# Kernel tuning notes

Hardware: AMD Instinct MI355X
Metric: run time of the kernel (lower is better)

## Reference

```python
import jax, jax.numpy as jnp
import numpy as np

B, NS, S, H = 512, 2, 128, 768
DS, NL = 384, 40
TEMP, ALPHA, GAMMA = 0.05, 0.15, 7.5
EPS = 1e-8


def setup_inputs() -> dict:
    key = jax.random.key(0)
    ks = jax.random.split(key, 8)
    return {
        "bert_emb": jax.random.normal(ks[0], (B, NS, S, H), dtype=jnp.float32),
        "rel_desc_emb": jax.random.normal(ks[1], (B, DS), dtype=jnp.float32),
        "dense_w": 0.02 * jax.random.normal(ks[2], (H, H), dtype=jnp.float32),
        "dense_b": jnp.zeros((H,), dtype=jnp.float32),
        "cls_w": 0.02 * jax.random.normal(ks[3], (3 * H, NL), dtype=jnp.float32),
        "cls_b": jnp.zeros((NL,), dtype=jnp.float32),
        "fc_w": 0.02 * jax.random.normal(ks[4], (3 * H, DS), dtype=jnp.float32),
        "fc_b": jnp.zeros((DS,), dtype=jnp.float32),
        "entity_idx": jax.random.randint(ks[5], (B, NS, 2), 0, S, dtype=jnp.int64 if jax.config.jax_enable_x64 else jnp.int32),
        "classify_labels": jax.random.randint(ks[6], (B,), 0, NL, dtype=jnp.int64 if jax.config.jax_enable_x64 else jnp.int32),
    }


def _mean_ce(logits, labels):
    lp = jax.nn.log_softmax(logits, axis=-1)
    return -jnp.mean(jnp.take_along_axis(lp, labels[:, None], axis=1))


def _l2n(x):
    return x / jnp.maximum(jnp.linalg.norm(x, axis=-1, keepdims=True), EPS)


def reference(bert_emb, rel_desc_emb, dense_w, dense_b, cls_w, cls_b, fc_w, fc_b,
              entity_idx, classify_labels):
    b = bert_emb.shape[0]
    bidx = jnp.arange(b)
    # ----- relation representation from sentence 0 (cls | head | tail) -----
    s0 = bert_emb[:, 0]                                   # [B,S,H]
    cls_tok = s0[:, 0]                                    # [B,H]
    head = s0[bidx, entity_idx[:, 0, 0]]                  # [B,H]
    tail = s0[bidx, entity_idx[:, 0, 1]]                  # [B,H]
    relation_hidden = jnp.tanh(jnp.concatenate([cls_tok, head, tail], axis=-1))  # [B,3H]
    logits = relation_hidden @ cls_w + cls_b              # [B,NL]
    ce_loss = _mean_ce(logits, classify_labels)
    # ----- margin loss vs relation-description embeddings (cosine) -----
    rel_emb = relation_hidden @ fc_w + fc_b               # [B,DS]
    C = _l2n(rel_emb) @ _l2n(rel_desc_emb).T              # [B,B] cosine sims
    pos = jnp.diagonal(C)
    diff_label = classify_labels[:, None] != classify_labels[None, :]
    neg = jnp.max(jnp.where(diff_label, C, -jnp.inf), axis=1)
    neg = jnp.maximum(neg, 0.0)                           # max_val initialized at 0
    margin_loss = jnp.sum(jax.nn.relu(neg - pos + GAMMA)) * (1.0 - ALPHA)
    ce_loss = ce_loss + margin_loss
    # ----- contrastive loss on (head|tail) entity pairs from both sents -----
    # dense is token-wise; apply only to the 4 gathered tokens per example
    h1a = bert_emb[bidx, 0, entity_idx[:, 0, 0]]
    h1b = bert_emb[bidx, 0, entity_idx[:, 0, 1]]
    h2a = bert_emb[bidx, 1, entity_idx[:, 1, 0]]
    h2b = bert_emb[bidx, 1, entity_idx[:, 1, 1]]
    toks = jnp.stack([h1a, h1b, h2a, h2b], axis=1)        # [B,4,H]
    toks = jnp.tanh(toks @ dense_w + dense_b)             # [B,4,H]
    z1 = toks[:, 0:2].reshape(b, -1)                      # [B,2H]
    z2 = toks[:, 2:4].reshape(b, -1)                      # [B,2H]
    cos_sim = (_l2n(z1) @ _l2n(z2).T) / TEMP              # [B,B]
    cl_loss = _mean_ce(cos_sim, bidx)
    return ce_loss + ALPHA * cl_loss
```

## Files before the change

### kernel.cpp

```cpp
#include <hip/hip_runtime.h>
#include <hip/hip_bf16.h>
#include <math.h>

#define B_   512
#define NS_  2
#define S_   128
#define H_   768
#define DS_  384
#define NL_  40
#define H3_  (3*H_)
#define TEMP_ 0.05f
#define ALPHA_ 0.15f
#define GAMMA_ 7.5f
#define EPS_ 1e-8f

typedef __attribute__((ext_vector_type(8))) short bf8_t;
typedef __attribute__((ext_vector_type(4))) float f4_t;

#define LDSPAD 40


__device__ __forceinline__ float block_reduce_sum(float v, float* sh) {
    int t = threadIdx.x;
    sh[t] = v; __syncthreads();
    for (int s = blockDim.x / 2; s > 0; s >>= 1) {
        if (t < s) sh[t] += sh[t + s];
        __syncthreads();
    }
    float r = sh[0]; __syncthreads();
    return r;
}

__device__ __forceinline__ float block_reduce_max(float v, float* sh) {
    int t = threadIdx.x;
    sh[t] = v; __syncthreads();
    for (int s = blockDim.x / 2; s > 0; s >>= 1) {
        if (t < s) sh[t] = fmaxf(sh[t], sh[t + s]);
        __syncthreads();
    }
    float r = sh[0]; __syncthreads();
    return r;
}

__device__ __forceinline__ void transpose_tile(
    const float* __restrict__ in, __hip_bfloat16* __restrict__ out,
    int K, int N, int kt, int nt, int tid, float* tileLds )
{
    int k0 = kt * 32, n0 = nt * 32;
    int tx = tid & 31, ty = tid >> 5;
#pragma unroll
    for (int i = 0; i < 4; ++i) {
        int k = k0 + ty + i * 8, n = n0 + tx;
        if (k < K && n < N) tileLds[(ty + i*8) * 33 + tx] = in[(size_t)k * N + n];
    }
    __syncthreads();
#pragma unroll
    for (int i = 0; i < 4; ++i) {
        int n = n0 + ty + i * 8, k = k0 + tx;
        if (n < N && k < K) out[(size_t)n * K + k] = __float2bfloat16(tileLds[tx * 33 + ty + i*8]);
    }
}

__global__ __launch_bounds__(256) void prep_kernel(
    const float* __restrict__ bert, const int* __restrict__ eidx,
    const float* __restrict__ dense_w, const float* __restrict__ fc_w,
    const float* __restrict__ cls_w, const float* __restrict__ desc,
    __hip_bfloat16* __restrict__ rh_bf, __hip_bfloat16* __restrict__ toks_bf,
    __hip_bfloat16* __restrict__ dwt, __hip_bfloat16* __restrict__ fwt,
    __hip_bfloat16* __restrict__ cwt, __hip_bfloat16* __restrict__ desc_nb,
    float* __restrict__ acc, int* __restrict__ done)
{
    __shared__ float tileLds[32 * 33];
    int blk = blockIdx.x;
    int t = threadIdx.x;
    if (blk < 512) {
        int b = blk;
        if (b == 0) {
            if (t < 4) acc[t] = 0.0f;
            if (t == 4) *done = 0;
        }
        int e00 = eidx[b*4 + 0];
        int e01 = eidx[b*4 + 1];
        int e10 = eidx[b*4 + 2];
        int e11 = eidx[b*4 + 3];
        const float* s0 = bert + (size_t)b * NS_ * S_ * H_;
        const float* s1 = s0 + (size_t)S_ * H_;
        const float* cls  = s0;
        const float* head = s0 + (size_t)e00 * H_;
        const float* tail = s0 + (size_t)e01 * H_;
        const float* h2a  = s1 + (size_t)e10 * H_;
        const float* h2b  = s1 + (size_t)e11 * H_;
        __hip_bfloat16* rhb = rh_bf + (size_t)b * H3_;
        __hip_bfloat16* tk  = toks_bf + (size_t)b * 4 * H_;
        for (int h = t; h < H_; h += 256) {
            float c  = cls[h];
            float hd = head[h];
            float tl = tail[h];
            rhb[h]        = __float2bfloat16(tanhf(c));
            rhb[H_ + h]   = __float2bfloat16(tanhf(hd));
            rhb[2*H_ + h] = __float2bfloat16(tanhf(tl));
            tk[h]         = __float2bfloat16(hd);
            tk[H_ + h]    = __float2bfloat16(tl);
            tk[2*H_ + h]  = __float2bfloat16(h2a[h]);
            tk[3*H_ + h]  = __float2bfloat16(h2b[h]);
        }
    } else if (blk < 1088) {
        int q = blk - 512;
        transpose_tile(dense_w, dwt, H_, H_, q / 24, q % 24, t, tileLds);
    } else if (blk < 1952) {
        int q = blk - 1088;
        transpose_tile(fc_w, fwt, H3_, DS_, q / 12, q % 12, t, tileLds);
    } else if (blk < 2096) {
        int q = blk - 1952;
        int kt = q / 2, nt = q % 2;
        transpose_tile(cls_w, cwt, H3_, NL_, kt, nt, t, tileLds);
        if (nt == 1) {
            int tx = t & 31, ty = t >> 5;
            cwt[(size_t)(40 + ty) * H3_ + kt * 32 + tx] = __float2bfloat16(0.0f);
        }
    } else {
        int i = blk - 2096;
        const float* x = desc + (size_t)i * DS_;
        float ss = 0.0f;
        for (int d = t; d < DS_; d += 256) { float v = x[d]; ss += v * v; }
        ss = block_reduce_sum(ss, tileLds);
        float inv = 1.0f / fmaxf(sqrtf(ss), EPS_);
        __hip_bfloat16* o = desc_nb + (size_t)i * DS_;
        for (int d = t; d < DS_; d += 256) o[d] = __float2bfloat16(x[d] * inv);
    }
}


__device__ __forceinline__ void gemm128_body(
    const __hip_bfloat16* __restrict__ A, const __hip_bfloat16* __restrict__ Bp,
    const float* __restrict__ bias, float* __restrict__ C,
    int K, int lda, int ldb, int ldc, int fuse_tanh, int bx, int by,
    __hip_bfloat16* As, __hip_bfloat16* Bs)
{
    int tid  = threadIdx.x;
    int lane = tid & 63;
    int wave = tid >> 6;
    int wm = (wave >> 1) * 64;
    int wn = (wave & 1) * 64;
    int lr = lane & 15;
    int quad = lane >> 4;
    int rowBase = by * 128;
    int colBase = bx * 128;

    f4_t acc[4][4];
#pragma unroll
    for (int i = 0; i < 4; ++i)
#pragma unroll
        for (int j = 0; j < 4; ++j) acc[i][j] = (f4_t){0.f, 0.f, 0.f, 0.f};

    int sr = tid >> 2, sc = tid & 3;
    for (int k0 = 0; k0 < K; k0 += 32) {
#pragma unroll
        for (int half = 0; half < 2; ++half) {
            int r = sr + half * 64;
            *(bf8_t*)&As[r * LDSPAD + sc * 8] =
                *(const bf8_t*)(A + (size_t)(rowBase + r) * lda + k0 + sc * 8);
            *(bf8_t*)&Bs[r * LDSPAD + sc * 8] =
                *(const bf8_t*)(Bp + (size_t)(colBase + r) * ldb + k0 + sc * 8);
        }
        __syncthreads();
        bf8_t af[4], bfr[4];
#pragma unroll
        for (int f = 0; f < 4; ++f) {
            af[f]  = *(const bf8_t*)&As[(wm + f*16 + lr) * LDSPAD + quad * 8];
            bfr[f] = *(const bf8_t*)&Bs[(wn + f*16 + lr) * LDSPAD + quad * 8];
        }
#pragma unroll
        for (int i = 0; i < 4; ++i)
#pragma unroll
            for (int j = 0; j < 4; ++j)
                acc[i][j] = __builtin_amdgcn_mfma_f32_16x16x32_bf16(af[i], bfr[j], acc[i][j], 0, 0, 0);
        __syncthreads();
    }
#pragma unroll
    for (int j = 0; j < 4; ++j) {
        int col = colBase + wn + j*16 + lr;
        float bv = bias ? bias[col] : 0.0f;
#pragma unroll
        for (int i = 0; i < 4; ++i) {
            int row0 = rowBase + wm + i*16 + quad*4;
#pragma unroll
            for (int r = 0; r < 4; ++r) {
                float v = acc[i][j][r] + bv;
                if (fuse_tanh) v = tanhf(v);
                C[(size_t)(row0 + r) * ldc + col] = v;
            }
        }
    }
}

__device__ __forceinline__ void gemm64_body(
    const __hip_bfloat16* __restrict__ A, const __hip_bfloat16* __restrict__ Bp,
    const float* __restrict__ bias, float* __restrict__ C,
    int K, int lda, int ldb, int ldc, float scale, int bx, int by,
    __hip_bfloat16* As, __hip_bfloat16* Bs)
{
    int tid  = threadIdx.x;
    int lane = tid & 63;
    int wave = tid >> 6;
    int lr = lane & 15;
    int quad = lane >> 4;
    int rowBase = by * 64;
    int colBase = bx * 64;

    f4_t acc[4];
#pragma unroll
    for (int i = 0; i < 4; ++i) acc[i] = (f4_t){0.f, 0.f, 0.f, 0.f};

    int sr = tid >> 2, sc = tid & 3;
    for (int k0 = 0; k0 < K; k0 += 32) {
        *(bf8_t*)&As[sr * LDSPAD + sc * 8] =
            *(const bf8_t*)(A + (size_t)(rowBase + sr) * lda + k0 + sc * 8);
        *(bf8_t*)&Bs[sr * LDSPAD + sc * 8] =
            *(const bf8_t*)(Bp + (size_t)(colBase + sr) * ldb + k0 + sc * 8);
        __syncthreads();
        bf8_t bfr = *(const bf8_t*)&Bs[(wave*16 + lr) * LDSPAD + quad * 8];
#pragma unroll
        for (int f = 0; f < 4; ++f) {
            bf8_t af = *(const bf8_t*)&As[(f*16 + lr) * LDSPAD + quad * 8];
            acc[f] = __builtin_amdgcn_mfma_f32_16x16x32_bf16(af, bfr, acc[f], 0, 0, 0);
        }
        __syncthreads();
    }
    int col = colBase + wave*16 + lr;
    float bv = bias ? bias[col] : 0.0f;
#pragma unroll
    for (int f = 0; f < 4; ++f) {
        int row0 = rowBase + f*16 + quad*4;
#pragma unroll
        for (int r = 0; r < 4; ++r)
            C[(size_t)(row0 + r) * ldc + col] = acc[f][r] * scale + bv;
    }
}

__device__ __forceinline__ void cls_ce_body(
    const __hip_bfloat16* __restrict__ rh, const __hip_bfloat16* __restrict__ cwt,
    const float* __restrict__ cls_b, const int* __restrict__ labels,
    float* __restrict__ acc, int rowBase, float* lgp )
{
    int tid  = threadIdx.x;
    int lane = tid & 63;
    int wave = tid >> 6;
    int lr = lane & 15;
    int quad = lane >> 4;

    f4_t a3[3];
#pragma unroll
    for (int j = 0; j < 3; ++j) a3[j] = (f4_t){0.f, 0.f, 0.f, 0.f};

    int kw0 = wave * (H3_ / 4);
    const __hip_bfloat16* aRow = rh + (size_t)(rowBase + lr) * H3_ + quad * 8;
#pragma unroll 2
    for (int s = 0; s < 18; ++s) {
        int k = kw0 + s * 32;
        bf8_t af = *(const bf8_t*)(aRow + k);
#pragma unroll
        for (int j = 0; j < 3; ++j) {
            bf8_t bfr = *(const bf8_t*)(cwt + (size_t)(j*16 + lr) * H3_ + k + quad * 8);
            a3[j] = __builtin_amdgcn_mfma_f32_16x16x32_bf16(af, bfr, a3[j], 0, 0, 0);
        }
    }
#pragma unroll
    for (int j = 0; j < 3; ++j) {
        int col = j*16 + lr;
#pragma unroll
        for (int r = 0; r < 4; ++r)
            lgp[wave * 768 + (quad*4 + r) * 48 + col] = a3[j][r];
    }
    __syncthreads();
    for (int idx = tid; idx < 768; idx += 256) {
        int col = idx % 48;
        float s = lgp[idx] + lgp[768 + idx] + lgp[1536 + idx] + lgp[2304 + idx];
        s = (col < NL_) ? (s + cls_b[col]) : -INFINITY;
        lgp[idx] = s;
    }
    __syncthreads();
    if (tid < 64) {
        float ce = 0.0f;
        if (tid < 16) {
            const float* Lr = &lgp[tid * 48];
            float m = -INFINITY;
            for (int c = 0; c < NL_; ++c) m = fmaxf(m, Lr[c]);
            float s = 0.0f;
            for (int c = 0; c < NL_; ++c) s += expf(Lr[c] - m);
            ce = logf(s) + m - Lr[labels[rowBase + tid]];
        }
        for (int off = 8; off >= 1; off >>= 1) ce += __shfl_down(ce, off);
        if (tid == 0) atomicAdd(acc + 0, ce * (1.0f / (float)B_));
    }
}

__global__ __launch_bounds__(256) void gemms_kernel(
    const __hip_bfloat16* __restrict__ toks_bf, const __hip_bfloat16* __restrict__ dwt,
    const float* __restrict__ dense_b, float* __restrict__ toks_out,
    const __hip_bfloat16* __restrict__ rh_bf, const __hip_bfloat16* __restrict__ fwt,
    const float* __restrict__ fc_b, float* __restrict__ rel_emb,
    const __hip_bfloat16* __restrict__ cwt, const float* __restrict__ cls_b,
    const int* __restrict__ labels, float* __restrict__ acc)
{
    __shared__ __align__(16) char smem[2 * 128 * LDSPAD * 2];
    int blk = blockIdx.x;
    if (blk < 96) {
        gemm128_body(toks_bf, dwt, dense_b, toks_out, H_, H_, H_, H_, 1,
                     blk % 6, blk / 6,
                     (__hip_bfloat16*)smem, (__hip_bfloat16*)(smem + 128 * LDSPAD * 2));
    } else if (blk < 144) {
        int q = blk - 96;
        gemm64_body(rh_bf, fwt, fc_b, rel_emb, H3_, H3_, H3_, DS_, 1.0f,
                    q % 6, q / 6,
                    (__hip_bfloat16*)smem, (__hip_bfloat16*)(smem + 64 * LDSPAD * 2));
    } else {
        cls_ce_body(rh_bf, cwt, cls_b, labels, acc, (blk - 144) * 16, (float*)smem);
    }
}

__global__ __launch_bounds__(256) void znorm_kernel(
    const float* __restrict__ rel_emb, const float* __restrict__ toks_out,
    __hip_bfloat16* __restrict__ rel_nb, __hip_bfloat16* __restrict__ z_bf)
{
    __shared__ float sh[256];
    int blk = blockIdx.x, t = threadIdx.x;
    const float* x; __hip_bfloat16* o; int D;
    if (blk < 512) { x = rel_emb + (size_t)blk * DS_;          o = rel_nb + (size_t)blk * DS_;        D = DS_; }
    else           { x = toks_out + (size_t)(blk-512) * 2*H_;  o = z_bf + (size_t)(blk-512) * 2*H_;   D = 2*H_; }
    float ss = 0.0f;
    for (int d = t; d < D; d += 256) { float v = x[d]; ss += v * v; }
    ss = block_reduce_sum(ss, sh);
    float inv = 1.0f / fmaxf(sqrtf(ss), EPS_);
    for (int d = t; d < D; d += 256) o[d] = __float2bfloat16(x[d] * inv);
}

__global__ __launch_bounds__(256) void c1c2_kernel(
    const __hip_bfloat16* __restrict__ rel_nb, const __hip_bfloat16* __restrict__ desc_nb,
    const __hip_bfloat16* __restrict__ z_bf, float* __restrict__ C1, float* __restrict__ C2)
{
    __shared__ __align__(16) char smem[2 * 64 * LDSPAD * 2];
    __hip_bfloat16* As = (__hip_bfloat16*)smem;
    __hip_bfloat16* Bs = (__hip_bfloat16*)(smem + 64 * LDSPAD * 2);
    int blk = blockIdx.x;
    if (blk < 64) {
        gemm64_body(rel_nb, desc_nb, (const float*)nullptr, C1, DS_, DS_, DS_, B_, 1.0f,
                    blk % 8, blk / 8, As, Bs);
    } else {
        int q = blk - 64;
        gemm64_body(z_bf, z_bf + 2*H_, (const float*)nullptr, C2, 2*H_, 4*H_, 4*H_, B_, 1.0f/TEMP_,
                    q % 8, q / 8, As, Bs);
    }
}

__global__ __launch_bounds__(256) void tail_kernel(
    const float* __restrict__ C1, const float* __restrict__ C2,
    const int* __restrict__ labels, float* __restrict__ acc,
    int* __restrict__ done, float* __restrict__ out)
{
    __shared__ float sh[256];
    int blk = blockIdx.x, t = threadIdx.x;
    if (blk < 512) {
        int i = blk;
        int li = labels[i];
        const float* row = C1 + (size_t)i * B_;
        float m = -INFINITY;
        for (int j = t; j < B_; j += 256)
            if (labels[j] != li) m = fmaxf(m, row[j]);
        float negmax = block_reduce_max(m, sh);
        if (t == 0) {
            float neg = fmaxf(negmax, 0.0f);
            float term = neg - row[i] + GAMMA_;
            if (term > 0.0f) atomicAdd(acc + 1, term);
        }
    } else {
        int i = blk - 512;
        const float* row = C2 + (size_t)i * B_;
        float m = -INFINITY;
        for (int j = t; j < B_; j += 256) m = fmaxf(m, row[j]);
        m = block_reduce_max(m, sh);
        float s = 0.0f;
        for (int j = t; j < B_; j += 256) s += expf(row[j] - m);
        s = block_reduce_sum(s, sh);
        if (t == 0) atomicAdd(acc + 2, (logf(s) + m - row[i]) * (1.0f / (float)B_));
    }
    __threadfence();
    if (t == 0) {
        int prev = atomicAdd(done, 1);
        if (prev == 1023) {
            float a0 = atomicAdd(acc + 0, 0.0f);
            float a1 = atomicAdd(acc + 1, 0.0f);
            float a2 = atomicAdd(acc + 2, 0.0f);
            out[0] = a0 + (1.0f - ALPHA_) * a1 + ALPHA_ * a2;
        }
    }
}


extern "C" void kernel_launch(void* const* d_in, const int* in_sizes, int n_in,
                              void* d_out, int out_size, void* d_ws, size_t ws_size,
                              hipStream_t stream) {
    const float* bert     = (const float*)d_in[0];
    const float* desc     = (const float*)d_in[1];
    const float* dense_w  = (const float*)d_in[2];
    const float* dense_b  = (const float*)d_in[3];
    const float* cls_w    = (const float*)d_in[4];
    const float* cls_b    = (const float*)d_in[5];
    const float* fc_w     = (const float*)d_in[6];
    const float* fc_b     = (const float*)d_in[7];
    const int*   eidx     = (const int*)d_in[8];
    const int*   labels   = (const int*)d_in[9];
    float* out = (float*)d_out;

    float* fp = (float*)d_ws;
    __hip_bfloat16* rh_bf   = (__hip_bfloat16*)fp; fp += (size_t)B_*H3_/2;
    __hip_bfloat16* toks_bf = (__hip_bfloat16*)fp; fp += (size_t)B_*4*H_/2;
    __hip_bfloat16* dwt_bf  = (__hip_bfloat16*)fp; fp += (size_t)H_*H_/2;
    __hip_bfloat16* fwt_bf  = (__hip_bfloat16*)fp; fp += (size_t)DS_*H3_/2;
    __hip_bfloat16* cwt_bf  = (__hip_bfloat16*)fp; fp += (size_t)48*H3_/2;
    __hip_bfloat16* desc_nb = (__hip_bfloat16*)fp; fp += (size_t)B_*DS_/2;
    __hip_bfloat16* rel_nb  = (__hip_bfloat16*)fp; fp += (size_t)B_*DS_/2;
    __hip_bfloat16* z_bf    = (__hip_bfloat16*)fp; fp += (size_t)B_*4*H_/2;
    float* toks_out = fp; fp += (size_t)B_*4*H_;
    float* rel_emb  = fp; fp += (size_t)B_*DS_;
    float* C1       = fp; fp += (size_t)B_*B_;
    float* C2       = fp; fp += (size_t)B_*B_;
    float* acc      = fp; fp += 4;
    int*   done     = (int*)fp;

    prep_kernel<<<2608, 256, 0, stream>>>(bert, eidx, dense_w, fc_w, cls_w, desc,
                                          rh_bf, toks_bf, dwt_bf, fwt_bf, cwt_bf,
                                          desc_nb, acc, done);

    gemms_kernel<<<176, 256, 0, stream>>>(toks_bf, dwt_bf, dense_b, toks_out,
                                          rh_bf, fwt_bf, fc_b, rel_emb,
                                          cwt_bf, cls_b, labels, acc);

    znorm_kernel<<<1536, 256, 0, stream>>>(rel_emb, toks_out, rel_nb, z_bf);

    c1c2_kernel<<<128, 256, 0, stream>>>(rel_nb, desc_nb, z_bf, C1, C2);

    tail_kernel<<<1024, 256, 0, stream>>>(C1, C2, labels, acc, done, out);
}
```

Baseline: 569.9 us.

## Fuse row-norm computation into GEMM epilogues and drop znorm kernel

The dense and fc GEMM epilogues now write bf16 outputs directly and accumulate per-row sums of squares with atomics. The similarity GEMMs then apply the inverse norms in their epilogue. This removes the separate normalization kernel, one launch, and the fp32 intermediate round-trip through memory. In exchange it adds atomic traffic and normalizes after the bf16 rounding rather than before it.

```diff
diff --git a/kernel.cpp b/kernel.cpp
--- a/kernel.cpp
+++ b/kernel.cpp
@@ -42,6 +42,18 @@
     return r;
 }
 
+__device__ __forceinline__ float quadgroup_reduce(float v) {
+    v += __shfl_down(v, 8);
+    v += __shfl_down(v, 4);
+    v += __shfl_down(v, 2);
+    v += __shfl_down(v, 1);
+    return v;
+}
+
+__device__ __forceinline__ float inv_norm(float ssq) {
+    return 1.0f / fmaxf(sqrtf(ssq), EPS_);
+}
+
 __device__ __forceinline__ void transpose_tile(
     const float* __restrict__ in, __hip_bfloat16* __restrict__ out,
     int K, int N, int kt, int nt, int tid, float* tileLds )
@@ -68,6 +80,7 @@
     __hip_bfloat16* __restrict__ rh_bf, __hip_bfloat16* __restrict__ toks_bf,
     __hip_bfloat16* __restrict__ dwt, __hip_bfloat16* __restrict__ fwt,
     __hip_bfloat16* __restrict__ cwt, __hip_bfloat16* __restrict__ desc_nb,
+    float* __restrict__ relssq, float* __restrict__ zssq,
     float* __restrict__ acc, int* __restrict__ done)
 {
     __shared__ float tileLds[32 * 33];
@@ -76,6 +89,8 @@
     if (blk < 512) {
         int b = blk;
         if (b == 0) {
+            for (int i = t; i < 512; i += 256) relssq[i] = 0.0f;
+            for (int i = t; i < 1024; i += 256) zssq[i] = 0.0f;
             if (t < 4) acc[t] = 0.0f;
             if (t == 4) *done = 0;
         }
@@ -124,17 +139,16 @@
         float ss = 0.0f;
         for (int d = t; d < DS_; d += 256) { float v = x[d]; ss += v * v; }
         ss = block_reduce_sum(ss, tileLds);
-        float inv = 1.0f / fmaxf(sqrtf(ss), EPS_);
+        float inv = inv_norm(ss);
         __hip_bfloat16* o = desc_nb + (size_t)i * DS_;
         for (int d = t; d < DS_; d += 256) o[d] = __float2bfloat16(x[d] * inv);
     }
 }
 
-
-__device__ __forceinline__ void gemm128_body(
+__device__ __forceinline__ void dense_body(
     const __hip_bfloat16* __restrict__ A, const __hip_bfloat16* __restrict__ Bp,
-    const float* __restrict__ bias, float* __restrict__ C,
-    int K, int lda, int ldb, int ldc, int fuse_tanh, int bx, int by,
+    const float* __restrict__ bias, __hip_bfloat16* __restrict__ toks_z,
+    float* __restrict__ zssq, int bx, int by,
     __hip_bfloat16* As, __hip_bfloat16* Bs)
 {
     int tid  = threadIdx.x;
@@ -154,14 +168,14 @@
         for (int j = 0; j < 4; ++j) acc[i][j] = (f4_t){0.f, 0.f, 0.f, 0.f};
 
     int sr = tid >> 2, sc = tid & 3;
-    for (int k0 = 0; k0 < K; k0 += 32) {
+    for (int k0 = 0; k0 < H_; k0 += 32) {
 #pragma unroll
         for (int half = 0; half < 2; ++half) {
             int r = sr + half * 64;
             *(bf8_t*)&As[r * LDSPAD + sc * 8] =
-                *(const bf8_t*)(A + (size_t)(rowBase + r) * lda + k0 + sc * 8);
+                *(const bf8_t*)(A + (size_t)(rowBase + r) * H_ + k0 + sc * 8);
             *(bf8_t*)&Bs[r * LDSPAD + sc * 8] =
-                *(const bf8_t*)(Bp + (size_t)(colBase + r) * ldb + k0 + sc * 8);
+                *(const bf8_t*)(Bp + (size_t)(colBase + r) * H_ + k0 + sc * 8);
         }
         __syncthreads();
         bf8_t af[4], bfr[4];
@@ -177,27 +191,34 @@
                 acc[i][j] = __builtin_amdgcn_mfma_f32_16x16x32_bf16(af[i], bfr[j], acc[i][j], 0, 0, 0);
         __syncthreads();
     }
-#pragma unroll
-    for (int j = 0; j < 4; ++j) {
-        int col = colBase + wn + j*16 + lr;
-        float bv = bias ? bias[col] : 0.0f;
-#pragma unroll
-        for (int i = 0; i < 4; ++i) {
-            int row0 = rowBase + wm + i*16 + quad*4;
-#pragma unroll
-            for (int r = 0; r < 4; ++r) {
-                float v = acc[i][j][r] + bv;
-                if (fuse_tanh) v = tanhf(v);
-                C[(size_t)(row0 + r) * ldc + col] = v;
+    float bv[4];
+#pragma unroll
+    for (int j = 0; j < 4; ++j) bv[j] = bias[colBase + wn + j*16 + lr];
+#pragma unroll
+    for (int i = 0; i < 4; ++i) {
+#pragma unroll
+        for (int r = 0; r < 4; ++r) {
+            int row = rowBase + wm + i*16 + quad*4 + r;
+            float s = 0.0f;
+#pragma unroll
+            for (int j = 0; j < 4; ++j) {
+                float v = tanhf(acc[i][j][r] + bv[j]);
+                toks_z[(size_t)row * H_ + colBase + wn + j*16 + lr] = __float2bfloat16(v);
+                s += v * v;
             }
-        }
-    }
-}
-
-__device__ __forceinline__ void gemm64_body(
+            s = quadgroup_reduce(s);
+            if (lr == 0) {
+                int zrow = (row >> 2) * 2 + ((row & 3) >> 1);
+                atomicAdd(&zssq[zrow], s);
+            }
+        }
+    }
+}
+
+__device__ __forceinline__ void fc_body(
     const __hip_bfloat16* __restrict__ A, const __hip_bfloat16* __restrict__ Bp,
-    const float* __restrict__ bias, float* __restrict__ C,
-    int K, int lda, int ldb, int ldc, float scale, int bx, int by,
+    const float* __restrict__ bias, __hip_bfloat16* __restrict__ rel_bf,
+    float* __restrict__ relssq, int bx, int by,
     __hip_bfloat16* As, __hip_bfloat16* Bs)
 {
     int tid  = threadIdx.x;
@@ -213,11 +234,11 @@
     for (int i = 0; i < 4; ++i) acc[i] = (f4_t){0.f, 0.f, 0.f, 0.f};
 
     int sr = tid >> 2, sc = tid & 3;
-    for (int k0 = 0; k0 < K; k0 += 32) {
+    for (int k0 = 0; k0 < H3_; k0 += 32) {
         *(bf8_t*)&As[sr * LDSPAD + sc * 8] =
-            *(const bf8_t*)(A + (size_t)(rowBase + sr) * lda + k0 + sc * 8);
+            *(const bf8_t*)(A + (size_t)(rowBase + sr) * H3_ + k0 + sc * 8);
         *(bf8_t*)&Bs[sr * LDSPAD + sc * 8] =
-            *(const bf8_t*)(Bp + (size_t)(colBase + sr) * ldb + k0 + sc * 8);
+            *(const bf8_t*)(Bp + (size_t)(colBase + sr) * H3_ + k0 + sc * 8);
         __syncthreads();
         bf8_t bfr = *(const bf8_t*)&Bs[(wave*16 + lr) * LDSPAD + quad * 8];
 #pragma unroll
@@ -228,13 +249,17 @@
         __syncthreads();
     }
     int col = colBase + wave*16 + lr;
-    float bv = bias ? bias[col] : 0.0f;
+    float bv = bias[col];
 #pragma unroll
     for (int f = 0; f < 4; ++f) {
-        int row0 = rowBase + f*16 + quad*4;
-#pragma unroll
-        for (int r = 0; r < 4; ++r)
-            C[(size_t)(row0 + r) * ldc + col] = acc[f][r] * scale + bv;
+#pragma unroll
+        for (int r = 0; r < 4; ++r) {
+            int row = rowBase + f*16 + quad*4 + r;
+            float v = acc[f][r] + bv;
+            rel_bf[(size_t)row * DS_ + col] = __float2bfloat16(v);
+            float s = quadgroup_reduce(v * v);
+            if (lr == 0) atomicAdd(&relssq[row], s);
+        }
     }
 }
 
@@ -297,59 +322,93 @@
 
 __global__ __launch_bounds__(256) void gemms_kernel(
     const __hip_bfloat16* __restrict__ toks_bf, const __hip_bfloat16* __restrict__ dwt,
-    const float* __restrict__ dense_b, float* __restrict__ toks_out,
+    const float* __restrict__ dense_b, __hip_bfloat16* __restrict__ toks_z,
     const __hip_bfloat16* __restrict__ rh_bf, const __hip_bfloat16* __restrict__ fwt,
-    const float* __restrict__ fc_b, float* __restrict__ rel_emb,
+    const float* __restrict__ fc_b, __hip_bfloat16* __restrict__ rel_bf,
     const __hip_bfloat16* __restrict__ cwt, const float* __restrict__ cls_b,
-    const int* __restrict__ labels, float* __restrict__ acc)
+    const int* __restrict__ labels, float* __restrict__ relssq,
+    float* __restrict__ zssq, float* __restrict__ acc)
 {
     __shared__ __align__(16) char smem[2 * 128 * LDSPAD * 2];
     int blk = blockIdx.x;
     if (blk < 96) {
-        gemm128_body(toks_bf, dwt, dense_b, toks_out, H_, H_, H_, H_, 1,
-                     blk % 6, blk / 6,
-                     (__hip_bfloat16*)smem, (__hip_bfloat16*)(smem + 128 * LDSPAD * 2));
+        dense_body(toks_bf, dwt, dense_b, toks_z, zssq, blk % 6, blk / 6,
+                   (__hip_bfloat16*)smem, (__hip_bfloat16*)(smem + 128 * LDSPAD * 2));
     } else if (blk < 144) {
         int q = blk - 96;
-        gemm64_body(rh_bf, fwt, fc_b, rel_emb, H3_, H3_, H3_, DS_, 1.0f,
-                    q % 6, q / 6,
-                    (__hip_bfloat16*)smem, (__hip_bfloat16*)(smem + 64 * LDSPAD * 2));
+        fc_body(rh_bf, fwt, fc_b, rel_bf, relssq, q % 6, q / 6,
+                (__hip_bfloat16*)smem, (__hip_bfloat16*)(smem + 64 * LDSPAD * 2));
     } else {
         cls_ce_body(rh_bf, cwt, cls_b, labels, acc, (blk - 144) * 16, (float*)smem);
     }
 }
 
-__global__ __launch_bounds__(256) void znorm_kernel(
-    const float* __restrict__ rel_emb, const float* __restrict__ toks_out,
-    __hip_bfloat16* __restrict__ rel_nb, __hip_bfloat16* __restrict__ z_bf)
-{
-    __shared__ float sh[256];
-    int blk = blockIdx.x, t = threadIdx.x;
-    const float* x; __hip_bfloat16* o; int D;
-    if (blk < 512) { x = rel_emb + (size_t)blk * DS_;          o = rel_nb + (size_t)blk * DS_;        D = DS_; }
-    else           { x = toks_out + (size_t)(blk-512) * 2*H_;  o = z_bf + (size_t)(blk-512) * 2*H_;   D = 2*H_; }
-    float ss = 0.0f;
-    for (int d = t; d < D; d += 256) { float v = x[d]; ss += v * v; }
-    ss = block_reduce_sum(ss, sh);
-    float inv = 1.0f / fmaxf(sqrtf(ss), EPS_);
-    for (int d = t; d < D; d += 256) o[d] = __float2bfloat16(x[d] * inv);
+__device__ __forceinline__ void sim_body(
+    const __hip_bfloat16* __restrict__ A, const __hip_bfloat16* __restrict__ Bp,
+    float* __restrict__ C, int K, int lda, int ldb,
+    const float* __restrict__ rssq, const float* __restrict__ cssq,
+    int rstride, int roff, int cstride, int coff, float scale,
+    int bx, int by, __hip_bfloat16* As, __hip_bfloat16* Bs)
+{
+    int tid  = threadIdx.x;
+    int lane = tid & 63;
+    int wave = tid >> 6;
+    int lr = lane & 15;
+    int quad = lane >> 4;
+    int rowBase = by * 64;
+    int colBase = bx * 64;
+
+    f4_t acc[4];
+#pragma unroll
+    for (int i = 0; i < 4; ++i) acc[i] = (f4_t){0.f, 0.f, 0.f, 0.f};
+
+    int sr = tid >> 2, sc = tid & 3;
+    for (int k0 = 0; k0 < K; k0 += 32) {
+        *(bf8_t*)&As[sr * LDSPAD + sc * 8] =
+            *(const bf8_t*)(A + (size_t)(rowBase + sr) * lda + k0 + sc * 8);
+        *(bf8_t*)&Bs[sr * LDSPAD + sc * 8] =
+            *(const bf8_t*)(Bp + (size_t)(colBase + sr) * ldb + k0 + sc * 8);
+        __syncthreads();
+        bf8_t bfr = *(const bf8_t*)&Bs[(wave*16 + lr) * LDSPAD + quad * 8];
+#pragma unroll
+        for (int f = 0; f < 4; ++f) {
+            bf8_t af = *(const bf8_t*)&As[(f*16 + lr) * LDSPAD + quad * 8];
+            acc[f] = __builtin_amdgcn_mfma_f32_16x16x32_bf16(af, bfr, acc[f], 0, 0, 0);
+        }
+        __syncthreads();
+    }
+    int col = colBase + wave*16 + lr;
+    float cinv = cssq ? inv_norm(cssq[col * cstride + coff]) : 1.0f;
+#pragma unroll
+    for (int f = 0; f < 4; ++f) {
+#pragma unroll
+        for (int r = 0; r < 4; ++r) {
+            int row = rowBase + f*16 + quad*4 + r;
+            float rinv = inv_norm(rssq[row * rstride + roff]);
+            C[(size_t)row * B_ + col] = acc[f][r] * rinv * cinv * scale;
+        }
+    }
 }
 
 __global__ __launch_bounds__(256) void c1c2_kernel(
-    const __hip_bfloat16* __restrict__ rel_nb, const __hip_bfloat16* __restrict__ desc_nb,
-    const __hip_bfloat16* __restrict__ z_bf, float* __restrict__ C1, float* __restrict__ C2)
+    const __hip_bfloat16* __restrict__ rel_bf, const __hip_bfloat16* __restrict__ desc_nb,
+    const __hip_bfloat16* __restrict__ toks_z,
+    const float* __restrict__ relssq, const float* __restrict__ zssq,
+    float* __restrict__ C1, float* __restrict__ C2)
 {
     __shared__ __align__(16) char smem[2 * 64 * LDSPAD * 2];
     __hip_bfloat16* As = (__hip_bfloat16*)smem;
     __hip_bfloat16* Bs = (__hip_bfloat16*)(smem + 64 * LDSPAD * 2);
     int blk = blockIdx.x;
     if (blk < 64) {
-        gemm64_body(rel_nb, desc_nb, (const float*)nullptr, C1, DS_, DS_, DS_, B_, 1.0f,
-                    blk % 8, blk / 8, As, Bs);
+        sim_body(rel_bf, desc_nb, C1, DS_, DS_, DS_,
+                 relssq, (const float*)nullptr, 1, 0, 0, 0, 1.0f,
+                 blk % 8, blk / 8, As, Bs);
     } else {
         int q = blk - 64;
-        gemm64_body(z_bf, z_bf + 2*H_, (const float*)nullptr, C2, 2*H_, 4*H_, 4*H_, B_, 1.0f/TEMP_,
-                    q % 8, q / 8, As, Bs);
+        sim_body(toks_z, toks_z + 2*H_, C2, 2*H_, 4*H_, 4*H_,
+                 zssq, zssq, 2, 0, 2, 1, 1.0f / TEMP_,
+                 q % 8, q / 8, As, Bs);
     }
 }
 
@@ -419,26 +478,24 @@
     __hip_bfloat16* fwt_bf  = (__hip_bfloat16*)fp; fp += (size_t)DS_*H3_/2;
     __hip_bfloat16* cwt_bf  = (__hip_bfloat16*)fp; fp += (size_t)48*H3_/2;
     __hip_bfloat16* desc_nb = (__hip_bfloat16*)fp; fp += (size_t)B_*DS_/2;
-    __hip_bfloat16* rel_nb  = (__hip_bfloat16*)fp; fp += (size_t)B_*DS_/2;
-    __hip_bfloat16* z_bf    = (__hip_bfloat16*)fp; fp += (size_t)B_*4*H_/2;
-    float* toks_out = fp; fp += (size_t)B_*4*H_;
-    float* rel_emb  = fp; fp += (size_t)B_*DS_;
+    __hip_bfloat16* toks_z  = (__hip_bfloat16*)fp; fp += (size_t)B_*4*H_/2;
+    __hip_bfloat16* rel_bf  = (__hip_bfloat16*)fp; fp += (size_t)B_*DS_/2;
     float* C1       = fp; fp += (size_t)B_*B_;
     float* C2       = fp; fp += (size_t)B_*B_;
+    float* relssq   = fp; fp += 512;
+    float* zssq     = fp; fp += 1024;
     float* acc      = fp; fp += 4;
     int*   done     = (int*)fp;
 
     prep_kernel<<<2608, 256, 0, stream>>>(bert, eidx, dense_w, fc_w, cls_w, desc,
                                           rh_bf, toks_bf, dwt_bf, fwt_bf, cwt_bf,
-                                          desc_nb, acc, done);
-
-    gemms_kernel<<<176, 256, 0, stream>>>(toks_bf, dwt_bf, dense_b, toks_out,
-                                          rh_bf, fwt_bf, fc_b, rel_emb,
-                                          cwt_bf, cls_b, labels, acc);
-
-    znorm_kernel<<<1536, 256, 0, stream>>>(rel_emb, toks_out, rel_nb, z_bf);
-
-    c1c2_kernel<<<128, 256, 0, stream>>>(rel_nb, desc_nb, z_bf, C1, C2);
+                                          desc_nb, relssq, zssq, acc, done);
+
+    gemms_kernel<<<176, 256, 0, stream>>>(toks_bf, dwt_bf, dense_b, toks_z,
+                                          rh_bf, fwt_bf, fc_b, rel_bf,
+                                          cwt_bf, cls_b, labels, relssq, zssq, acc);
+
+    c1c2_kernel<<<128, 256, 0, stream>>>(rel_bf, desc_nb, toks_z, relssq, zssq, C1, C2);
 
     tail_kernel<<<1024, 256, 0, stream>>>(C1, C2, labels, acc, done, out);
 }
```

Result: no change. 575.9 us (+1.1%).
